# Optimization experiments

Measured on AMD Instinct MI355X. Metric: run time of the kernel, lower is better.

The kernel has to match this reference:

```python
import jax, jax.numpy as jnp
import numpy as np

B, H, W, C = 32, 32, 32, 512
HEADS, WS, SS = 16, 8, 4
N = WS * WS            # tokens per window
NW = (H // WS) * (W // WS)  # windows per image
HD = C // HEADS
EPS = 1e-5


def _np_window_partition(x, ws):
    b, h, w, c = x.shape
    x = x.reshape(b, h // ws, ws, w // ws, ws, c).transpose(0, 1, 3, 2, 4, 5)
    return x.reshape(-1, ws, ws, c)


def _make_attn_mask():
    img = np.zeros((1, H, W, 1), np.float32)
    sl = (slice(0, -WS), slice(-WS, -SS), slice(-SS, None))
    cnt = 0
    for hs in sl:
        for ws_ in sl:
            img[:, hs, ws_, :] = cnt
            cnt += 1
    mw = _np_window_partition(img, WS).reshape(-1, N)
    d = mw[:, None, :] - mw[:, :, None]
    return np.where(d != 0, np.float32(-100.0), np.float32(0.0))  # [nW, N, N]


def _rel_pos_index():
    coords = np.stack(np.meshgrid(np.arange(WS), np.arange(WS), indexing='ij'))  # [2,ws,ws]
    cf = coords.reshape(2, -1)
    rel = cf[:, :, None] - cf[:, None, :]          # [2,N,N]
    rel = rel.transpose(1, 2, 0)                    # [N,N,2]
    rel[:, :, 0] += WS - 1
    rel[:, :, 1] += WS - 1
    rel[:, :, 0] *= 2 * WS - 1
    return rel.sum(-1)                              # [N,N]

_ATTN_MASK = jnp.asarray(_make_attn_mask())
_RPI = jnp.asarray(_rel_pos_index())


def _ln(x, w, b):
    mu = jnp.mean(x, -1, keepdims=True)
    var = jnp.mean(jnp.square(x - mu), -1, keepdims=True)
    return (x - mu) * jax.lax.rsqrt(var + EPS) * w + b


def _modulate(x, shift, scale):
    return x * (1.0 + scale[:, None, :]) + shift[:, None, :]


def setup_inputs() -> dict:
    key = jax.random.key(0)
    ks = jax.random.split(key, 8)
    s = lambda fan: 1.0 / np.sqrt(fan)
    return {
        'x': jax.random.normal(ks[0], (B, H * W, C), jnp.float32),
        'cond': jax.random.normal(ks[1], (B, C), jnp.float32),
        'norm1_w': jnp.ones((C,), jnp.float32),
        'norm1_b': jnp.zeros((C,), jnp.float32),
        'qkv_w': jax.random.normal(ks[2], (3 * C, C), jnp.float32) * s(C),
        'qkv_b': jnp.zeros((3 * C,), jnp.float32),
        'rpb_table': jax.random.normal(ks[3], ((2 * WS - 1) ** 2, HEADS), jnp.float32) * 0.02,
        'proj_w': jax.random.normal(ks[4], (C, C), jnp.float32) * s(C),
        'proj_b': jnp.zeros((C,), jnp.float32),
        'norm2_w': jnp.ones((C,), jnp.float32),
        'norm2_b': jnp.zeros((C,), jnp.float32),
        'fc1_w': jax.random.normal(ks[5], (4 * C, C), jnp.float32) * s(C),
        'fc1_b': jnp.zeros((4 * C,), jnp.float32),
        'fc2_w': jax.random.normal(ks[6], (C, 4 * C), jnp.float32) * s(4 * C),
        'fc2_b': jnp.zeros((C,), jnp.float32),
        'ada_w': jax.random.normal(ks[7], (6 * C, C), jnp.float32) * s(C),
        'ada_b': jnp.zeros((6 * C,), jnp.float32),
    }


def reference(x, cond, norm1_w, norm1_b, qkv_w, qkv_b, rpb_table, proj_w, proj_b,
              norm2_w, norm2_b, fc1_w, fc1_b, fc2_w, fc2_b, ada_w, ada_b):
    # adaLN modulation params
    ada = jax.nn.silu(cond) @ ada_w.T + ada_b                      # [B, 6C]
    sh_msa, sc_msa, g_msa, sh_mlp, sc_mlp, g_mlp = jnp.split(ada, 6, axis=1)

    shortcut = x
    h = _modulate(_ln(x, norm1_w, norm1_b), sh_msa, sc_msa)        # [B, L, C]
    h = h.reshape(B, H, W, C)
    h = jnp.roll(h, shift=(-SS, -SS), axis=(1, 2))                 # cyclic shift

    # window partition -> [B*nW, N, C]
    hw = h.reshape(B, H // WS, WS, W // WS, WS, C).transpose(0, 1, 3, 2, 4, 5)
    hw = hw.reshape(B * NW, N, C)

    # window attention with relative position bias + shift mask
    qkv = (hw @ qkv_w.T + qkv_b).reshape(B * NW, N, 3, HEADS, HD)
    qkv = qkv.transpose(2, 0, 3, 1, 4)                             # [3, B_, heads, N, hd]
    q, k, v = qkv[0], qkv[1], qkv[2]
    attn = jnp.einsum('bhnd,bhmd->bhnm', q * (HD ** -0.5), k)      # [B_, heads, N, N]
    rpb = rpb_table[_RPI.reshape(-1)].reshape(N, N, HEADS).transpose(2, 0, 1)
    attn = attn + rpb[None]
    attn = attn.reshape(B, NW, HEADS, N, N) + _ATTN_MASK[None, :, None]
    attn = jax.nn.softmax(attn.reshape(B * NW, HEADS, N, N), axis=-1)
    out = jnp.einsum('bhnm,bhmd->bhnd', attn, v)                   # [B_, heads, N, hd]
    out = out.transpose(0, 2, 1, 3).reshape(B * NW, N, C)
    out = out @ proj_w.T + proj_b

    # window reverse -> [B, H, W, C]
    out = out.reshape(B, H // WS, W // WS, WS, WS, C).transpose(0, 1, 3, 2, 4, 5)
    out = out.reshape(B, H, W, C)
    out = jnp.roll(out, shift=(SS, SS), axis=(1, 2)).reshape(B, H * W, C)

    x = shortcut + g_msa[:, None, :] * out

    m = _modulate(_ln(x, norm2_w, norm2_b), sh_mlp, sc_mlp)
    m = jax.nn.gelu(m @ fc1_w.T + fc1_b, approximate=False) @ fc2_w.T + fc2_b
    return x + g_mlp[:, None, :] * m
```

## Files before the change

### kernel.cpp

```cpp
#include <hip/hip_runtime.h>
#include <math.h>

typedef unsigned short u16;
typedef short short8 __attribute__((ext_vector_type(8)));
typedef float floatx4 __attribute__((ext_vector_type(4)));

#define SS 4
#define C_DIM 512
#define L_TOK 1024

static __device__ __forceinline__ u16 f2bf(float f) {
  union { float f; unsigned u; } v; v.f = f;
  unsigned u = v.u;
  unsigned r = (u + 0x7fffu + ((u >> 16) & 1u)) >> 16;
  return (u16)r;
}

typedef const __attribute__((address_space(1))) void* gvp;
typedef __attribute__((address_space(3))) void* lvp;
#define ASYNC16(g, l) __builtin_amdgcn_global_load_lds((gvp)(g), (lvp)(l), 16, 0, 0)

__global__ __launch_bounds__(256) void convert_all(const float* __restrict__ s0,
                                                   const float* __restrict__ s1,
                                                   const float* __restrict__ s2,
                                                   const float* __restrict__ s3,
                                                   u16* __restrict__ d0, u16* __restrict__ d1,
                                                   u16* __restrict__ d2, u16* __restrict__ d3) {
  int i = blockIdx.x * 256 + threadIdx.x;
  const float* src; u16* dst; int off;
  if (i < 196608)      { src = s0; dst = d0; off = i; }
  else if (i < 262144) { src = s1; dst = d1; off = i - 196608; }
  else if (i < 524288) { src = s2; dst = d2; off = i - 262144; }
  else                 { src = s3; dst = d3; off = i - 524288; }
  float4 v = ((const float4*)src)[off];
  ushort4 o;
  o.x = f2bf(v.x); o.y = f2bf(v.y); o.z = f2bf(v.z); o.w = f2bf(v.w);
  ((ushort4*)dst)[off] = o;
}

__global__ __launch_bounds__(256) void ada_kernel(const float* __restrict__ cond,
                                                  const float* __restrict__ w,
                                                  const float* __restrict__ bias,
                                                  float* __restrict__ ada) {
  int b = blockIdx.y;
  int j = blockIdx.x * 256 + threadIdx.x;
  __shared__ float sc[C_DIM];
  for (int c = threadIdx.x; c < C_DIM; c += 256) {
    float v = cond[b * C_DIM + c];
    sc[c] = v / (1.0f + expf(-v));
  }
  __syncthreads();
  const float* wr = w + (size_t)j * C_DIM;
  float acc = 0.f;
  for (int k = 0; k < C_DIM; k += 4) {
    float4 wv = *(const float4*)&wr[k];
    acc += sc[k] * wv.x + sc[k + 1] * wv.y + sc[k + 2] * wv.z + sc[k + 3] * wv.w;
  }
  ada[(size_t)b * 3072 + j] = acc + bias[j];
}

__global__ __launch_bounds__(64) void prep_attn(const float* __restrict__ rpb,
                                                float* __restrict__ rpbT,
                                                unsigned long long* __restrict__ maskbits) {
  int q = blockIdx.x;
  int head = blockIdx.y;
  int k = threadIdx.x;
  int i1 = q >> 3, j1 = q & 7, i2 = k >> 3, j2 = k & 7;
  rpbT[((size_t)head * 64 + q) * 64 + k] =
      rpb[((i1 - i2 + 7) * 15 + (j1 - j2 + 7)) * 16 + head];
  if (head == 0) {
    for (int widx = 0; widx < 16; widx++) {
      int wh = widx >> 2, wwi = widx & 3;
      int hq = wh * 8 + i1, wq = wwi * 8 + j1;
      int hk = wh * 8 + i2, wk = wwi * 8 + j2;
      int rq = ((hq < 24) ? 0 : (hq < 28) ? 1 : 2) * 3 + ((wq < 24) ? 0 : (wq < 28) ? 1 : 2);
      int rk = ((hk < 24) ? 0 : (hk < 28) ? 1 : 2) * 3 + ((wk < 24) ? 0 : (wk < 28) ? 1 : 2);
      unsigned long long m = __ballot(rq != rk);
      if (k == 0) maskbits[widx * 64 + q] = m;
    }
  }
}

template <int MODE>
__global__ __launch_bounds__(128) void ln_mod(const float* __restrict__ x,
                                              const float* __restrict__ ada,
                                              const float* __restrict__ nw,
                                              const float* __restrict__ nb,
                                              u16* __restrict__ out) {
  int m = blockIdx.x;
  int b = m >> 10;
  size_t srow;
  if (MODE == 0) {
    int n = m & 63, widx = (m >> 6) & 15;
    int wh = widx >> 2, wwi = widx & 3;
    int i = n >> 3, j = n & 7;
    int hs = (wh * 8 + i + SS) & 31;
    int ws_ = (wwi * 8 + j + SS) & 31;
    srow = (size_t)b * L_TOK + hs * 32 + ws_;
  } else {
    srow = (size_t)m;
  }
  const float* src = x + srow * C_DIM;
  int t = threadIdx.x;
  float4 v = *(const float4*)&src[t * 4];
  float s = v.x + v.y + v.z + v.w;
  float ss = v.x * v.x + v.y * v.y + v.z * v.z + v.w * v.w;
#pragma unroll
  for (int off = 32; off > 0; off >>= 1) {
    s += __shfl_down(s, off);
    ss += __shfl_down(ss, off);
  }
  __shared__ float red[4];
  if ((t & 63) == 0) { red[(t >> 6) * 2] = s; red[(t >> 6) * 2 + 1] = ss; }
  __syncthreads();
  float mean = (red[0] + red[2]) * (1.f / C_DIM);
  float var = (red[1] + red[3]) * (1.f / C_DIM) - mean * mean;
  float rstd = rsqrtf(var + 1e-5f);
  const float* sh = ada + (size_t)b * 3072 + (MODE ? 1536 : 0);
  const float* scm = ada + (size_t)b * 3072 + (MODE ? 2048 : 512);
  int c = t * 4;
  ushort4 o;
  {
    float y;
    y = ((v.x - mean) * rstd * nw[c + 0] + nb[c + 0]) * (1.f + scm[c + 0]) + sh[c + 0]; o.x = f2bf(y);
    y = ((v.y - mean) * rstd * nw[c + 1] + nb[c + 1]) * (1.f + scm[c + 1]) + sh[c + 1]; o.y = f2bf(y);
    y = ((v.z - mean) * rstd * nw[c + 2] + nb[c + 2]) * (1.f + scm[c + 2]) + sh[c + 2]; o.z = f2bf(y);
    y = ((v.w - mean) * rstd * nw[c + 3] + nb[c + 3]) * (1.f + scm[c + 3]) + sh[c + 3]; o.w = f2bf(y);
  }
  *(ushort4*)&out[(size_t)m * C_DIM + c] = o;
}

template <int EPI>
__global__ __launch_bounds__(256, 2) void gemm_bf16(
    const u16* __restrict__ A, const u16* __restrict__ Bw,
    const float* __restrict__ bias, int K, int N,
    u16* __restrict__ outBf, float* __restrict__ outF,
    const float* __restrict__ resid, const float* __restrict__ ada) {
  __shared__ __align__(16) u16 lA[2][128 * 32];
  __shared__ __align__(16) u16 lB[2][128 * 32];
  const int tid = threadIdx.x;
  const int lane = tid & 63, wave = tid >> 6;
  const int wr = wave >> 1, wc = wave & 1;
  const int gx = gridDim.x;
  const int id = blockIdx.y * gx + blockIdx.x;
  const int per = (gx * gridDim.y) >> 3;
  const int nid = (id & 7) * per + (id >> 3);
  const int rowA0 = (nid / gx) * 128;
  const int colB0 = (nid % gx) * 128;
  floatx4 acc[4][4];
#pragma unroll
  for (int a = 0; a < 4; a++)
#pragma unroll
    for (int b = 0; b < 4; b++) acc[a][b] = (floatx4){0.f, 0.f, 0.f, 0.f};

  const int r0 = tid >> 2, c0 = (tid & 3) * 8;
  const int q = lane >> 4, fr = lane & 15;

  const u16* gA = &A[(size_t)(rowA0 + r0) * K + c0];
  const u16* gB = &Bw[(size_t)(colB0 + r0) * K + c0];
  const size_t up = (size_t)64 * K;
  u16* lA0 = &lA[0][wave * 512];
  u16* lB0 = &lB[0][wave * 512];

  for (int k0 = 0; k0 < K; k0 += 64) {
    ASYNC16(gA + k0, lA0);
    ASYNC16(gA + k0 + up, lA0 + 2048);
    ASYNC16(gA + k0 + 32, lA0 + 4096);
    ASYNC16(gA + k0 + 32 + up, lA0 + 6144);
    ASYNC16(gB + k0, lB0);
    ASYNC16(gB + k0 + up, lB0 + 2048);
    ASYNC16(gB + k0 + 32, lB0 + 4096);
    ASYNC16(gB + k0 + 32 + up, lB0 + 6144);
    __syncthreads();
#pragma unroll
    for (int kc = 0; kc < 2; kc++) {
      short8 xf[4], wf[4];
#pragma unroll
      for (int mi = 0; mi < 4; mi++)
        xf[mi] = *(const short8*)&lA[kc][(wr * 64 + mi * 16 + fr) * 32 + q * 8];
#pragma unroll
      for (int ni = 0; ni < 4; ni++)
        wf[ni] = *(const short8*)&lB[kc][(wc * 64 + ni * 16 + fr) * 32 + q * 8];
#pragma unroll
      for (int mi = 0; mi < 4; mi++)
#pragma unroll
        for (int ni = 0; ni < 4; ni++)
          acc[mi][ni] = __builtin_amdgcn_mfma_f32_16x16x32_bf16(wf[ni], xf[mi], acc[mi][ni], 0, 0, 0);
    }
    __syncthreads();
  }

#pragma unroll
  for (int mi = 0; mi < 4; mi++) {
    int row = rowA0 + wr * 64 + mi * 16 + fr;
#pragma unroll
    for (int ni = 0; ni < 4; ni++) {
      int col0 = colB0 + wc * 64 + ni * 16 + q * 4;
      float4 bv = *(const float4*)&bias[col0];
      float v0 = acc[mi][ni][0] + bv.x;
      float v1 = acc[mi][ni][1] + bv.y;
      float v2 = acc[mi][ni][2] + bv.z;
      float v3 = acc[mi][ni][3] + bv.w;
      if (EPI == 1) {
        v0 = __fdividef(v0, 1.f + __expf(-v0 * (1.59576912f + 0.07135481f * v0 * v0)));
        v1 = __fdividef(v1, 1.f + __expf(-v1 * (1.59576912f + 0.07135481f * v1 * v1)));
        v2 = __fdividef(v2, 1.f + __expf(-v2 * (1.59576912f + 0.07135481f * v2 * v2)));
        v3 = __fdividef(v3, 1.f + __expf(-v3 * (1.59576912f + 0.07135481f * v3 * v3)));
      }
      if (EPI == 0 || EPI == 1) {
        ushort4 pk;
        pk.x = f2bf(v0); pk.y = f2bf(v1); pk.z = f2bf(v2); pk.w = f2bf(v3);
        *(ushort4*)&outBf[(size_t)row * N + col0] = pk;
      } else if (EPI == 2) {
        int b = row >> 10;
        int n = row & 63, widx = (row >> 6) & 15;
        int wh = widx >> 2, wwi = widx & 3;
        int i = n >> 3, j = n & 7;
        int hd = (wh * 8 + i + SS) & 31;
        int wd = (wwi * 8 + j + SS) & 31;
        size_t dst = ((size_t)b * L_TOK + hd * 32 + wd) * C_DIM + col0;
        float4 rs = *(const float4*)&resid[dst];
        float4 g = *(const float4*)&ada[(size_t)b * 3072 + 1024 + col0];
        float4 o;
        o.x = rs.x + g.x * v0; o.y = rs.y + g.y * v1;
        o.z = rs.z + g.z * v2; o.w = rs.w + g.w * v3;
        *(float4*)&outF[dst] = o;
      } else {
        int b = row >> 10;
        size_t dst = (size_t)row * C_DIM + col0;
        float4 cur = *(const float4*)&outF[dst];
        float4 g = *(const float4*)&ada[(size_t)b * 3072 + 2560 + col0];
        float4 o;
        o.x = cur.x + g.x * v0; o.y = cur.y + g.y * v1;
        o.z = cur.z + g.z * v2; o.w = cur.w + g.w * v3;
        *(float4*)&outF[dst] = o;
      }
    }
  }
}

__global__ __launch_bounds__(64, 4) void attn_mfma(const u16* __restrict__ qkv,
                                                   const float* __restrict__ rpbT,
                                                   const unsigned long long* __restrict__ maskbits,
                                                   u16* __restrict__ out) {
  __shared__ __align__(16) u16 VT[32 * 72];
  __shared__ __align__(16) u16 P[64 * 72];
  const int lane = threadIdx.x;
  const int col = lane & 15, quad = lane >> 4;
  const int id = blockIdx.x;
  const int w_ = id >> 4, head = id & 15;
  const int widx = w_ & 15;
  const u16* base = qkv + (size_t)w_ * 64 * 1536 + head * 32;

  {
    const u16* vrow = base + 1024 + (size_t)lane * 1536;
#pragma unroll
    for (int c = 0; c < 4; c++) {
      uint4 u = *(const uint4*)&vrow[c * 8];
      unsigned uu0 = u.x, uu1 = u.y, uu2 = u.z, uu3 = u.w;
      VT[(c * 8 + 0) * 72 + lane] = (u16)(uu0 & 0xffff);
      VT[(c * 8 + 1) * 72 + lane] = (u16)(uu0 >> 16);
      VT[(c * 8 + 2) * 72 + lane] = (u16)(uu1 & 0xffff);
      VT[(c * 8 + 3) * 72 + lane] = (u16)(uu1 >> 16);
      VT[(c * 8 + 4) * 72 + lane] = (u16)(uu2 & 0xffff);
      VT[(c * 8 + 5) * 72 + lane] = (u16)(uu2 >> 16);
      VT[(c * 8 + 6) * 72 + lane] = (u16)(uu3 & 0xffff);
      VT[(c * 8 + 7) * 72 + lane] = (u16)(uu3 >> 16);
    }
  }

  short8 kf[4], qf[4];
#pragma unroll
  for (int mi = 0; mi < 4; mi++)
    kf[mi] = *(const short8*)(base + 512 + (size_t)(mi * 16 + col) * 1536 + quad * 8);
#pragma unroll
  for (int ni = 0; ni < 4; ni++)
    qf[ni] = *(const short8*)(base + (size_t)(ni * 16 + col) * 1536 + quad * 8);

  floatx4 st[4][4];
#pragma unroll
  for (int mi = 0; mi < 4; mi++)
#pragma unroll
    for (int ni = 0; ni < 4; ni++) st[mi][ni] = (floatx4){0.f, 0.f, 0.f, 0.f};
#pragma unroll
  for (int mi = 0; mi < 4; mi++)
#pragma unroll
    for (int ni = 0; ni < 4; ni++)
      st[mi][ni] = __builtin_amdgcn_mfma_f32_16x16x32_bf16(kf[mi], qf[ni], st[mi][ni], 0, 0, 0);

  const float scale = 0.17677669529663687f;
  float invq[4];
#pragma unroll
  for (int ni = 0; ni < 4; ni++) {
    int q = ni * 16 + col;
    unsigned long long mw = maskbits[widx * 64 + q];
    const float* rp = rpbT + ((size_t)head * 64 + q) * 64;
    float mx = -1e30f;
#pragma unroll
    for (int mi = 0; mi < 4; mi++) {
      floatx4 r4 = *(const floatx4*)&rp[mi * 16 + quad * 4];
#pragma unroll
      for (int r = 0; r < 4; r++) {
        int key = mi * 16 + quad * 4 + r;
        float s = st[mi][ni][r] * scale + r4[r];
        s -= ((mw >> key) & 1ull) ? 100.f : 0.f;
        st[mi][ni][r] = s;
        mx = fmaxf(mx, s);
      }
    }
    mx = fmaxf(mx, __shfl_xor(mx, 16));
    mx = fmaxf(mx, __shfl_xor(mx, 32));
    float sum = 0.f;
#pragma unroll
    for (int mi = 0; mi < 4; mi++) {
      float e0 = __expf(st[mi][ni][0] - mx);
      float e1 = __expf(st[mi][ni][1] - mx);
      float e2 = __expf(st[mi][ni][2] - mx);
      float e3 = __expf(st[mi][ni][3] - mx);
      sum += e0 + e1 + e2 + e3;
      ushort4 pk;
      pk.x = f2bf(e0); pk.y = f2bf(e1); pk.z = f2bf(e2); pk.w = f2bf(e3);
      *(ushort4*)&P[q * 72 + mi * 16 + quad * 4] = pk;
    }
    sum += __shfl_xor(sum, 16);
    sum += __shfl_xor(sum, 32);
    invq[ni] = 1.f / sum;
  }
  __syncthreads();

  floatx4 o[2][4];
#pragma unroll
  for (int mt = 0; mt < 2; mt++)
#pragma unroll
    for (int nt = 0; nt < 4; nt++) o[mt][nt] = (floatx4){0.f, 0.f, 0.f, 0.f};
#pragma unroll
  for (int kc = 0; kc < 2; kc++) {
    short8 vf0 = *(const short8*)&VT[(col) * 72 + kc * 32 + quad * 8];
    short8 vf1 = *(const short8*)&VT[(16 + col) * 72 + kc * 32 + quad * 8];
#pragma unroll
    for (int nt = 0; nt < 4; nt++) {
      short8 pf = *(const short8*)&P[(nt * 16 + col) * 72 + kc * 32 + quad * 8];
      o[0][nt] = __builtin_amdgcn_mfma_f32_16x16x32_bf16(vf0, pf, o[0][nt], 0, 0, 0);
      o[1][nt] = __builtin_amdgcn_mfma_f32_16x16x32_bf16(vf1, pf, o[1][nt], 0, 0, 0);
    }
  }

#pragma unroll
  for (int mt = 0; mt < 2; mt++)
#pragma unroll
    for (int nt = 0; nt < 4; nt++) {
      int q = nt * 16 + col;
      float iv = invq[nt];
      ushort4 pk;
      pk.x = f2bf(o[mt][nt][0] * iv);
      pk.y = f2bf(o[mt][nt][1] * iv);
      pk.z = f2bf(o[mt][nt][2] * iv);
      pk.w = f2bf(o[mt][nt][3] * iv);
      *(ushort4*)&out[((size_t)w_ * 64 + q) * 512 + head * 32 + mt * 16 + quad * 4] = pk;
    }
}

extern "C" void kernel_launch(void* const* d_in, const int* in_sizes, int n_in,
                              void* d_out, int out_size, void* d_ws, size_t ws_size,
                              hipStream_t stream) {
  const float* x      = (const float*)d_in[0];
  const float* cond   = (const float*)d_in[1];
  const float* n1w    = (const float*)d_in[2];
  const float* n1b    = (const float*)d_in[3];
  const float* qkv_w  = (const float*)d_in[4];
  const float* qkv_b  = (const float*)d_in[5];
  const float* rpb    = (const float*)d_in[6];
  const float* proj_w = (const float*)d_in[7];
  const float* proj_b = (const float*)d_in[8];
  const float* n2w    = (const float*)d_in[9];
  const float* n2b    = (const float*)d_in[10];
  const float* fc1_w  = (const float*)d_in[11];
  const float* fc1_b  = (const float*)d_in[12];
  const float* fc2_w  = (const float*)d_in[13];
  const float* fc2_b  = (const float*)d_in[14];
  const float* ada_w  = (const float*)d_in[15];
  const float* ada_b  = (const float*)d_in[16];
  float* out = (float*)d_out;
  char* ws = (char*)d_ws;

  u16*  qkvw_bf  = (u16*)(ws + 0);
  u16*  projw_bf = (u16*)(ws + 1572864);
  u16*  fc1w_bf  = (u16*)(ws + 2097152);
  u16*  fc2w_bf  = (u16*)(ws + 4194304);
  float* ada     = (float*)(ws + 6291456);
  float* rpbT    = (float*)(ws + 6684672);
  unsigned long long* maskb = (unsigned long long*)(ws + 6946816);
  u16*  hw       = (u16*)(ws + 6955008);
  u16*  qkvo     = (u16*)(ws + 40509440);
  u16*  attno    = (u16*)(ws + 141172736);
  u16*  mlp      = (u16*)(ws + 40509440);

  convert_all<<<3072, 256, 0, stream>>>(qkv_w, proj_w, fc1_w, fc2_w,
                                        qkvw_bf, projw_bf, fc1w_bf, fc2w_bf);
  prep_attn<<<dim3(64, 16), 64, 0, stream>>>(rpb, rpbT, maskb);

  ada_kernel<<<dim3(12, 32), 256, 0, stream>>>(cond, ada_w, ada_b, ada);
  ln_mod<0><<<32768, 128, 0, stream>>>(x, ada, n1w, n1b, hw);
  gemm_bf16<0><<<dim3(12, 256), 256, 0, stream>>>(hw, qkvw_bf, qkv_b, 512, 1536,
                                                  qkvo, nullptr, nullptr, nullptr);
  attn_mfma<<<8192, 64, 0, stream>>>(qkvo, rpbT, maskb, attno);
  gemm_bf16<2><<<dim3(4, 256), 256, 0, stream>>>(attno, projw_bf, proj_b, 512, 512,
                                                 nullptr, out, x, ada);
  ln_mod<1><<<32768, 128, 0, stream>>>(out, ada, n2w, n2b, hw);
  gemm_bf16<1><<<dim3(16, 256), 256, 0, stream>>>(hw, fc1w_bf, fc1_b, 512, 2048,
                                                  mlp, nullptr, nullptr, nullptr);
  gemm_bf16<3><<<dim3(4, 256), 256, 0, stream>>>(mlp, fc2w_bf, fc2_b, 2048, 512,
                                                 nullptr, out, nullptr, ada);
}
```

Baseline: 566.2 us.

## Switch GEMM to 32x32x16 MFMA with XOR-swizzled 64-wide LDS tiles

The bf16 GEMM now uses 32x32x16 MFMA instructions with a 2x2 grid of 16-float accumulators per wave, replacing the 4x4 grid of 16x16x32 MFMAs. The LDS tiles are stored as full 64-wide K rows with an XOR swizzle applied to the 16-byte chunk index on the global-to-LDS async copies, which should cut bank conflicts on the fragment reads. The epilogue is rewritten for the 32x32 output layout, and the per-row address math for the residual and gate is hoisted out of the column loop. Larger MFMAs mean fewer instructions and fewer LDS reads per FLOP, but the output stores now cover smaller contiguous chunks per lane.

```diff
diff --git a/kernel.cpp b/kernel.cpp
--- a/kernel.cpp
+++ b/kernel.cpp
@@ -4,6 +4,7 @@
 typedef unsigned short u16;
 typedef short short8 __attribute__((ext_vector_type(8)));
 typedef float floatx4 __attribute__((ext_vector_type(4)));
+typedef float floatx16 __attribute__((ext_vector_type(16)));
 
 #define SS 4
 #define C_DIM 512
@@ -136,8 +137,8 @@
     const float* __restrict__ bias, int K, int N,
     u16* __restrict__ outBf, float* __restrict__ outF,
     const float* __restrict__ resid, const float* __restrict__ ada) {
-  __shared__ __align__(16) u16 lA[2][128 * 32];
-  __shared__ __align__(16) u16 lB[2][128 * 32];
+  __shared__ __align__(16) u16 lA[128 * 64];
+  __shared__ __align__(16) u16 lB[128 * 64];
   const int tid = threadIdx.x;
   const int lane = tid & 63, wave = tid >> 6;
   const int wr = wave >> 1, wc = wave & 1;
@@ -147,93 +148,106 @@
   const int nid = (id & 7) * per + (id >> 3);
   const int rowA0 = (nid / gx) * 128;
   const int colB0 = (nid % gx) * 128;
-  floatx4 acc[4][4];
-#pragma unroll
-  for (int a = 0; a < 4; a++)
-#pragma unroll
-    for (int b = 0; b < 4; b++) acc[a][b] = (floatx4){0.f, 0.f, 0.f, 0.f};
-
-  const int r0 = tid >> 2, c0 = (tid & 3) * 8;
-  const int q = lane >> 4, fr = lane & 15;
-
-  const u16* gA = &A[(size_t)(rowA0 + r0) * K + c0];
-  const u16* gB = &Bw[(size_t)(colB0 + r0) * K + c0];
-  const size_t up = (size_t)64 * K;
-  u16* lA0 = &lA[0][wave * 512];
-  u16* lB0 = &lB[0][wave * 512];
+
+  floatx16 acc[2][2];
+#pragma unroll
+  for (int a = 0; a < 2; a++)
+#pragma unroll
+    for (int b = 0; b < 2; b++)
+#pragma unroll
+      for (int r = 0; r < 16; r++) acc[a][b][r] = 0.f;
+
+  const int srow = tid >> 3;
+  const int gsw = ((lane & 7) ^ (lane >> 3)) * 8;
+  const u16* gA = &A[(size_t)(rowA0 + srow) * K + gsw];
+  const u16* gB = &Bw[(size_t)(colB0 + srow) * K + gsw];
+  u16* lAw = &lA[wave * 512];
+  u16* lBw = &lB[wave * 512];
+  const size_t rb = (size_t)32 * K;
+
+  const int m = lane & 31, half = lane >> 5;
+  const int w7 = m & 7;
 
   for (int k0 = 0; k0 < K; k0 += 64) {
-    ASYNC16(gA + k0, lA0);
-    ASYNC16(gA + k0 + up, lA0 + 2048);
-    ASYNC16(gA + k0 + 32, lA0 + 4096);
-    ASYNC16(gA + k0 + 32 + up, lA0 + 6144);
-    ASYNC16(gB + k0, lB0);
-    ASYNC16(gB + k0 + up, lB0 + 2048);
-    ASYNC16(gB + k0 + 32, lB0 + 4096);
-    ASYNC16(gB + k0 + 32 + up, lB0 + 6144);
+    ASYNC16(gA + k0, lAw);
+    ASYNC16(gA + k0 + rb, lAw + 2048);
+    ASYNC16(gA + k0 + 2 * rb, lAw + 4096);
+    ASYNC16(gA + k0 + 3 * rb, lAw + 6144);
+    ASYNC16(gB + k0, lBw);
+    ASYNC16(gB + k0 + rb, lBw + 2048);
+    ASYNC16(gB + k0 + 2 * rb, lBw + 4096);
+    ASYNC16(gB + k0 + 3 * rb, lBw + 6144);
     __syncthreads();
 #pragma unroll
-    for (int kc = 0; kc < 2; kc++) {
-      short8 xf[4], wf[4];
-#pragma unroll
-      for (int mi = 0; mi < 4; mi++)
-        xf[mi] = *(const short8*)&lA[kc][(wr * 64 + mi * 16 + fr) * 32 + q * 8];
-#pragma unroll
-      for (int ni = 0; ni < 4; ni++)
-        wf[ni] = *(const short8*)&lB[kc][(wc * 64 + ni * 16 + fr) * 32 + q * 8];
-#pragma unroll
-      for (int mi = 0; mi < 4; mi++)
-#pragma unroll
-        for (int ni = 0; ni < 4; ni++)
-          acc[mi][ni] = __builtin_amdgcn_mfma_f32_16x16x32_bf16(wf[ni], xf[mi], acc[mi][ni], 0, 0, 0);
+    for (int s = 0; s < 4; s++) {
+      const int go = (((2 * s) | half) ^ w7) * 8;
+      short8 x0 = *(const short8*)&lA[(wr * 64 + m) * 64 + go];
+      short8 x1 = *(const short8*)&lA[(wr * 64 + 32 + m) * 64 + go];
+      short8 w0 = *(const short8*)&lB[(wc * 64 + m) * 64 + go];
+      short8 w1 = *(const short8*)&lB[(wc * 64 + 32 + m) * 64 + go];
+      acc[0][0] = __builtin_amdgcn_mfma_f32_32x32x16_bf16(w0, x0, acc[0][0], 0, 0, 0);
+      acc[0][1] = __builtin_amdgcn_mfma_f32_32x32x16_bf16(w1, x0, acc[0][1], 0, 0, 0);
+      acc[1][0] = __builtin_amdgcn_mfma_f32_32x32x16_bf16(w0, x1, acc[1][0], 0, 0, 0);
+      acc[1][1] = __builtin_amdgcn_mfma_f32_32x32x16_bf16(w1, x1, acc[1][1], 0, 0, 0);
     }
     __syncthreads();
   }
 
 #pragma unroll
-  for (int mi = 0; mi < 4; mi++) {
-    int row = rowA0 + wr * 64 + mi * 16 + fr;
-#pragma unroll
-    for (int ni = 0; ni < 4; ni++) {
-      int col0 = colB0 + wc * 64 + ni * 16 + q * 4;
-      float4 bv = *(const float4*)&bias[col0];
-      float v0 = acc[mi][ni][0] + bv.x;
-      float v1 = acc[mi][ni][1] + bv.y;
-      float v2 = acc[mi][ni][2] + bv.z;
-      float v3 = acc[mi][ni][3] + bv.w;
-      if (EPI == 1) {
-        v0 = __fdividef(v0, 1.f + __expf(-v0 * (1.59576912f + 0.07135481f * v0 * v0)));
-        v1 = __fdividef(v1, 1.f + __expf(-v1 * (1.59576912f + 0.07135481f * v1 * v1)));
-        v2 = __fdividef(v2, 1.f + __expf(-v2 * (1.59576912f + 0.07135481f * v2 * v2)));
-        v3 = __fdividef(v3, 1.f + __expf(-v3 * (1.59576912f + 0.07135481f * v3 * v3)));
-      }
-      if (EPI == 0 || EPI == 1) {
-        ushort4 pk;
-        pk.x = f2bf(v0); pk.y = f2bf(v1); pk.z = f2bf(v2); pk.w = f2bf(v3);
-        *(ushort4*)&outBf[(size_t)row * N + col0] = pk;
-      } else if (EPI == 2) {
-        int b = row >> 10;
-        int n = row & 63, widx = (row >> 6) & 15;
-        int wh = widx >> 2, wwi = widx & 3;
-        int i = n >> 3, j = n & 7;
-        int hd = (wh * 8 + i + SS) & 31;
-        int wd = (wwi * 8 + j + SS) & 31;
-        size_t dst = ((size_t)b * L_TOK + hd * 32 + wd) * C_DIM + col0;
-        float4 rs = *(const float4*)&resid[dst];
-        float4 g = *(const float4*)&ada[(size_t)b * 3072 + 1024 + col0];
-        float4 o;
-        o.x = rs.x + g.x * v0; o.y = rs.y + g.y * v1;
-        o.z = rs.z + g.z * v2; o.w = rs.w + g.w * v3;
-        *(float4*)&outF[dst] = o;
-      } else {
-        int b = row >> 10;
-        size_t dst = (size_t)row * C_DIM + col0;
-        float4 cur = *(const float4*)&outF[dst];
-        float4 g = *(const float4*)&ada[(size_t)b * 3072 + 2560 + col0];
-        float4 o;
-        o.x = cur.x + g.x * v0; o.y = cur.y + g.y * v1;
-        o.z = cur.z + g.z * v2; o.w = cur.w + g.w * v3;
-        *(float4*)&outF[dst] = o;
+  for (int mi = 0; mi < 2; mi++) {
+    const int row = rowA0 + wr * 64 + mi * 32 + m;
+    size_t dstrow;
+    const float* gvec = nullptr;
+    if (EPI == 2) {
+      int b = row >> 10;
+      int n = row & 63, widx = (row >> 6) & 15;
+      int wh = widx >> 2, wwi = widx & 3;
+      int i = n >> 3, j = n & 7;
+      int hd = (wh * 8 + i + SS) & 31;
+      int wd = (wwi * 8 + j + SS) & 31;
+      dstrow = ((size_t)b * L_TOK + hd * 32 + wd) * C_DIM;
+      gvec = ada + (size_t)b * 3072 + 1024;
+    } else if (EPI == 3) {
+      dstrow = (size_t)row * C_DIM;
+      gvec = ada + (size_t)(row >> 10) * 3072 + 2560;
+    }
+#pragma unroll
+    for (int ni = 0; ni < 2; ni++) {
+#pragma unroll
+      for (int a = 0; a < 4; a++) {
+        const int col0 = colB0 + wc * 64 + ni * 32 + a * 8 + half * 4;
+        float4 bv = *(const float4*)&bias[col0];
+        float v0 = acc[mi][ni][a * 4 + 0] + bv.x;
+        float v1 = acc[mi][ni][a * 4 + 1] + bv.y;
+        float v2 = acc[mi][ni][a * 4 + 2] + bv.z;
+        float v3 = acc[mi][ni][a * 4 + 3] + bv.w;
+        if (EPI == 1) {
+          v0 = __fdividef(v0, 1.f + __expf(-v0 * (1.59576912f + 0.07135481f * v0 * v0)));
+          v1 = __fdividef(v1, 1.f + __expf(-v1 * (1.59576912f + 0.07135481f * v1 * v1)));
+          v2 = __fdividef(v2, 1.f + __expf(-v2 * (1.59576912f + 0.07135481f * v2 * v2)));
+          v3 = __fdividef(v3, 1.f + __expf(-v3 * (1.59576912f + 0.07135481f * v3 * v3)));
+        }
+        if (EPI == 0 || EPI == 1) {
+          ushort4 pk;
+          pk.x = f2bf(v0); pk.y = f2bf(v1); pk.z = f2bf(v2); pk.w = f2bf(v3);
+          *(ushort4*)&outBf[(size_t)row * N + col0] = pk;
+        } else if (EPI == 2) {
+          size_t dst = dstrow + col0;
+          float4 rs = *(const float4*)&resid[dst];
+          float4 g = *(const float4*)&gvec[col0];
+          float4 o;
+          o.x = rs.x + g.x * v0; o.y = rs.y + g.y * v1;
+          o.z = rs.z + g.z * v2; o.w = rs.w + g.w * v3;
+          *(float4*)&outF[dst] = o;
+        } else {
+          size_t dst = dstrow + col0;
+          float4 cur = *(const float4*)&outF[dst];
+          float4 g = *(const float4*)&gvec[col0];
+          float4 o;
+          o.x = cur.x + g.x * v0; o.y = cur.y + g.y * v1;
+          o.z = cur.z + g.z * v2; o.w = cur.w + g.w * v3;
+          *(float4*)&outF[dst] = o;
+        }
       }
     }
   }
```

New measurement: 653.9 us. 1.16x slower.
